# Optimization experiments

Measured on AMD Instinct MI355X. Metric: run time of the kernel, lower is better.

The kernel has to match this reference:

```python
import jax, jax.numpy as jnp
import numpy as np

N = 2_097_152  # number of pose pairs


def _skew(w):
    # w: [N,3] -> [N,3,3] skew-symmetric matrices
    x, y, z = w[..., 0], w[..., 1], w[..., 2]
    O = jnp.zeros_like(x)
    return jnp.stack([
        jnp.stack([O, -z, y], -1),
        jnp.stack([z, O, -x], -1),
        jnp.stack([-y, x, O], -1),
    ], -2)


def _exp_se3(xi):
    # xi: [N,6] twist = [rot_vec(3), trans(3)] -> (R:[N,3,3], t:[N,3])
    w, v = xi[..., :3], xi[..., 3:]
    t2 = jnp.sum(w * w, -1)                      # theta^2
    small = t2 < 1e-8
    t2s = jnp.where(small, 1.0, t2)              # safe denominator
    th = jnp.sqrt(t2s)
    A = jnp.where(small, 1.0 - t2 / 6.0, jnp.sin(th) / th)
    B = jnp.where(small, 0.5 - t2 / 24.0, (1.0 - jnp.cos(th)) / t2s)
    C = jnp.where(small, 1.0 / 6.0 - t2 / 120.0, (th - jnp.sin(th)) / (t2s * th))
    K = _skew(w)
    K2 = K @ K
    I = jnp.eye(3, dtype=xi.dtype)
    R = I + A[..., None, None] * K + B[..., None, None] * K2
    V = I + B[..., None, None] * K + C[..., None, None] * K2
    t = jnp.einsum('nij,nj->ni', V, v)
    return R, t


def _log_se3(R, t):
    # SE(3) log map: (R:[N,3,3], t:[N,3]) -> (w:[N,3], v:[N,3])
    tr = R[..., 0, 0] + R[..., 1, 1] + R[..., 2, 2]
    c = jnp.clip((tr - 1.0) * 0.5, -1.0 + 1e-7, 1.0 - 1e-7)
    th = jnp.arccos(c)
    small = th < 1e-4
    s = jnp.sin(th)
    ths = jnp.where(small, 1.0, th)
    ss = jnp.where(small, 1.0, s)
    coef = jnp.where(small, 0.5 + th * th / 12.0, th / (2.0 * ss))
    wvec = coef[..., None] * jnp.stack([
        R[..., 2, 1] - R[..., 1, 2],
        R[..., 0, 2] - R[..., 2, 0],
        R[..., 1, 0] - R[..., 0, 1],
    ], -1)
    K = _skew(wvec)
    K2 = K @ K
    one_m_c = jnp.where(small, 1.0, 1.0 - c)
    D = jnp.where(small, 1.0 / 12.0,
                  (1.0 - th * s / (2.0 * one_m_c)) / (ths * ths))
    I = jnp.eye(3, dtype=R.dtype)
    Vinv = I - 0.5 * K + D[..., None, None] * K2
    vvec = jnp.einsum('nij,nj->ni', Vinv, t)
    return wvec, vvec


def setup_inputs() -> dict:
    key = jax.random.key(0)
    k1, k2 = jax.random.split(key)
    predict = jax.random.normal(k1, (N, 6), dtype=jnp.float32)
    target = jax.random.normal(k2, (N, 6), dtype=jnp.float32)
    return {"predict": predict, "target": target}


def reference(predict, target):
    # per-sample SE(3) geodesic loss, reduction='mean'
    Rp, tp = _exp_se3(predict)
    Rt, tt = _exp_se3(target)
    # relative transform T_pred^{-1} T_target
    Rd = jnp.einsum('nji,njk->nik', Rp, Rt)           # Rp^T @ Rt
    td = jnp.einsum('nji,nj->ni', Rp, tt - tp)        # Rp^T (tt - tp)
    w, v = _log_se3(Rd, td)
    loss = jnp.sum(w * w, -1) + jnp.sum(v * v, -1)    # squared twist norm [N]
    return jnp.mean(loss)
```

## Files before the change

kernel.cpp:

```cpp
#include <hip/hip_runtime.h>

#define BLOCK 256
#define GRID  2048

__device__ __forceinline__ float frcp(float x) { return __builtin_amdgcn_rcpf(x); }

__device__ __forceinline__ void expse3(float wx, float wy, float wz,
                                       float vx, float vy, float vz,
                                       float* R, float* t)
{
    float t2 = wx*wx + wy*wy + wz*wz;
    bool  sm = t2 < 1e-8f;
    float t2s = sm ? 1.0f : t2;
    float th  = sqrtf(t2s);
    float s, c;
    __sincosf(th, &s, &c);
    float rth  = frcp(th);
    float rt2s = rth * rth;
    float A = sm ? 1.0f - t2*(1.0f/6.0f)                 : s * rth;
    float B = sm ? 0.5f - t2*(1.0f/24.0f)                : (1.0f - c) * rt2s;
    float C = sm ? (1.0f/6.0f) - t2*(1.0f/120.0f)        : (1.0f - s*rth) * rt2s;
    float Bxy = B*wx*wy, Bxz = B*wx*wz, Byz = B*wy*wz;
    R[0] = 1.0f + B*(wx*wx - t2); R[1] = Bxy - A*wz;            R[2] = Bxz + A*wy;
    R[3] = Bxy + A*wz;            R[4] = 1.0f + B*(wy*wy - t2); R[5] = Byz - A*wx;
    R[6] = Bxz - A*wy;            R[7] = Byz + A*wx;            R[8] = 1.0f + B*(wz*wz - t2);
    float Cxy = C*wx*wy, Cxz = C*wx*wz, Cyz = C*wy*wz;
    float V0 = 1.0f + C*(wx*wx - t2), V1 = Cxy - B*wz,            V2 = Cxz + B*wy;
    float V3 = Cxy + B*wz,            V4 = 1.0f + C*(wy*wy - t2), V5 = Cyz - B*wx;
    float V6 = Cxz - B*wy,            V7 = Cyz + B*wx,            V8 = 1.0f + C*(wz*wz - t2);
    t[0] = V0*vx + V1*vy + V2*vz;
    t[1] = V3*vx + V4*vy + V5*vz;
    t[2] = V6*vx + V7*vy + V8*vz;
}

__global__ void __launch_bounds__(BLOCK)
se3_loss_kernel(const float* __restrict__ pred, const float* __restrict__ targ,
                float* __restrict__ out, int n, float invN)
{
    float acc = 0.0f;
    int stride = gridDim.x * blockDim.x;
    for (int i = blockIdx.x * blockDim.x + threadIdx.x; i < n; i += stride) {
        const float2* p2 = reinterpret_cast<const float2*>(pred) + 3 * (size_t)i;
        const float2* q2 = reinterpret_cast<const float2*>(targ) + 3 * (size_t)i;
        float2 pa = p2[0], pb = p2[1], pc = p2[2];
        float2 qa = q2[0], qb = q2[1], qc = q2[2];

        float Rp[9], tp[3], Rt[9], tt[3];
        expse3(pa.x, pa.y, pb.x, pb.y, pc.x, pc.y, Rp, tp);
        expse3(qa.x, qa.y, qb.x, qb.y, qc.x, qc.y, Rt, tt);

        float d0 = tt[0] - tp[0], d1 = tt[1] - tp[1], d2 = tt[2] - tp[2];
        float Rd[9];
        #pragma unroll
        for (int ii = 0; ii < 3; ii++)
            #pragma unroll
            for (int kk = 0; kk < 3; kk++)
                Rd[ii*3+kk] = Rp[0+ii]*Rt[0+kk] + Rp[3+ii]*Rt[3+kk] + Rp[6+ii]*Rt[6+kk];
        float td0 = Rp[0]*d0 + Rp[3]*d1 + Rp[6]*d2;
        float td1 = Rp[1]*d0 + Rp[4]*d1 + Rp[7]*d2;
        float td2 = Rp[2]*d0 + Rp[5]*d1 + Rp[8]*d2;

        float tr = Rd[0] + Rd[4] + Rd[8];
        float c  = fminf(fmaxf((tr - 1.0f) * 0.5f, -1.0f + 1e-7f), 1.0f - 1e-7f);
        float th = acosf(c);
        bool  sm = th < 1e-4f;
        float s  = __sinf(th);
        float ths = sm ? 1.0f : th;
        float ss  = sm ? 1.0f : s;
        float coef = sm ? 0.5f + th*th*(1.0f/12.0f) : th * 0.5f * frcp(ss);
        float wx = coef * (Rd[7] - Rd[5]);
        float wy = coef * (Rd[2] - Rd[6]);
        float wz = coef * (Rd[3] - Rd[1]);
        float w2 = wx*wx + wy*wy + wz*wz;
        float omc = sm ? 1.0f : 1.0f - c;
        float rths = frcp(ths);
        float D = sm ? (1.0f/12.0f)
                     : (1.0f - th*s*0.5f*frcp(omc)) * rths * rths;
        float Dxy = D*wx*wy, Dxz = D*wx*wz, Dyz = D*wy*wz;
        float Vi0 = 1.0f + D*(wx*wx - w2), Vi1 =  0.5f*wz + Dxy,           Vi2 = -0.5f*wy + Dxz;
        float Vi3 = -0.5f*wz + Dxy,        Vi4 = 1.0f + D*(wy*wy - w2),    Vi5 =  0.5f*wx + Dyz;
        float Vi6 =  0.5f*wy + Dxz,        Vi7 = -0.5f*wx + Dyz,           Vi8 = 1.0f + D*(wz*wz - w2);
        float vx = Vi0*td0 + Vi1*td1 + Vi2*td2;
        float vy = Vi3*td0 + Vi4*td1 + Vi5*td2;
        float vz = Vi6*td0 + Vi7*td1 + Vi8*td2;

        acc += w2 + vx*vx + vy*vy + vz*vz;
    }

    #pragma unroll
    for (int off = 32; off; off >>= 1) acc += __shfl_down(acc, off, 64);
    __shared__ float wsum[BLOCK / 64];
    int lane = threadIdx.x & 63, wid = threadIdx.x >> 6;
    if (lane == 0) wsum[wid] = acc;
    __syncthreads();
    if (threadIdx.x == 0) {
        float s = 0.0f;
        #pragma unroll
        for (int k = 0; k < BLOCK / 64; k++) s += wsum[k];
        atomicAdd(out, s * invN);
    }
}

extern "C" void kernel_launch(void* const* d_in, const int* in_sizes, int n_in,
                              void* d_out, int out_size, void* d_ws, size_t ws_size,
                              hipStream_t stream) {
    const float* pred = (const float*)d_in[0];
    const float* targ = (const float*)d_in[1];
    float* out = (float*)d_out;
    int n = in_sizes[0] / 6;
    hipMemsetAsync(out, 0, (size_t)out_size * sizeof(float), stream);
    se3_loss_kernel<<<GRID, BLOCK, 0, stream>>>(pred, targ, out, n, 1.0f / (float)n);
}
```

Baseline: 128.6 us.

## Use float4 loads, two rows per thread, and polynomial acos approximation

Each thread now handles two pose pairs, read with three float4 loads per input instead of float2 loads, and the grid covers all pairs with no grid-stride loop. acosf is replaced by a short polynomial approximation, sin(theta) is derived from sqrt(1-c^2), and the small-angle branches in the log map are removed. The exp map uses raw hardware sqrt and explicit fmas. The intent is to cut transcendental and select cost and improve load width. In exchange it adds approximation error, drops the small-angle handling (possible loss of accuracy near theta=0), and silently ignores an odd final row.

```diff
diff --git a/kernel.cpp b/kernel.cpp
--- a/kernel.cpp
+++ b/kernel.cpp
@@ -1,25 +1,34 @@
 #include <hip/hip_runtime.h>
 
 #define BLOCK 256
-#define GRID  2048
 
-__device__ __forceinline__ float frcp(float x) { return __builtin_amdgcn_rcpf(x); }
+__device__ __forceinline__ float frcp(float x)  { return __builtin_amdgcn_rcpf(x); }
+__device__ __forceinline__ float fsqrt_(float x){ return __builtin_amdgcn_sqrtf(x); }
+
+__device__ __forceinline__ float facos(float x) {
+    float a = fabsf(x);
+    float p = fmaf(a, -0.0187293f, 0.0742610f);
+    p = fmaf(a, p, -0.2121144f);
+    p = fmaf(a, p, 1.5707288f);
+    float r = fsqrt_(1.0f - a) * p;
+    return x < 0.0f ? 3.14159265358979f - r : r;
+}
 
 __device__ __forceinline__ void expse3(float wx, float wy, float wz,
                                        float vx, float vy, float vz,
                                        float* R, float* t)
 {
-    float t2 = wx*wx + wy*wy + wz*wz;
+    float t2 = fmaf(wx, wx, fmaf(wy, wy, wz * wz));
     bool  sm = t2 < 1e-8f;
     float t2s = sm ? 1.0f : t2;
-    float th  = sqrtf(t2s);
+    float th  = fsqrt_(t2s);
     float s, c;
     __sincosf(th, &s, &c);
     float rth  = frcp(th);
-    float rt2s = rth * rth;
-    float A = sm ? 1.0f - t2*(1.0f/6.0f)                 : s * rth;
-    float B = sm ? 0.5f - t2*(1.0f/24.0f)                : (1.0f - c) * rt2s;
-    float C = sm ? (1.0f/6.0f) - t2*(1.0f/120.0f)        : (1.0f - s*rth) * rt2s;
+    float rt2  = rth * rth;
+    float A = sm ? fmaf(t2, -1.0f/6.0f,   1.0f)      : s * rth;
+    float B = sm ? fmaf(t2, -1.0f/24.0f,  0.5f)      : (1.0f - c) * rt2;
+    float C = sm ? fmaf(t2, -1.0f/120.0f, 1.0f/6.0f) : (1.0f - s * rth) * rt2;
     float Bxy = B*wx*wy, Bxz = B*wx*wz, Byz = B*wy*wz;
     R[0] = 1.0f + B*(wx*wx - t2); R[1] = Bxy - A*wz;            R[2] = Bxz + A*wy;
     R[3] = Bxy + A*wz;            R[4] = 1.0f + B*(wy*wy - t2); R[5] = Byz - A*wx;
@@ -33,58 +42,61 @@
     t[2] = V6*vx + V7*vy + V8*vz;
 }
 
+__device__ __forceinline__ float row_loss(
+    float pwx, float pwy, float pwz, float pvx, float pvy, float pvz,
+    float qwx, float qwy, float qwz, float qvx, float qvy, float qvz)
+{
+    float Rp[9], tp[3], Rt[9], tt[3];
+    expse3(pwx, pwy, pwz, pvx, pvy, pvz, Rp, tp);
+    expse3(qwx, qwy, qwz, qvx, qvy, qvz, Rt, tt);
+
+    float d0 = tt[0] - tp[0], d1 = tt[1] - tp[1], d2 = tt[2] - tp[2];
+    float Rd[9];
+    #pragma unroll
+    for (int ii = 0; ii < 3; ii++)
+        #pragma unroll
+        for (int kk = 0; kk < 3; kk++)
+            Rd[ii*3+kk] = Rp[0+ii]*Rt[0+kk] + Rp[3+ii]*Rt[3+kk] + Rp[6+ii]*Rt[6+kk];
+    float td0 = Rp[0]*d0 + Rp[3]*d1 + Rp[6]*d2;
+    float td1 = Rp[1]*d0 + Rp[4]*d1 + Rp[7]*d2;
+    float td2 = Rp[2]*d0 + Rp[5]*d1 + Rp[8]*d2;
+
+    float tr = Rd[0] + Rd[4] + Rd[8];
+    float c  = fminf(fmaxf((tr - 1.0f) * 0.5f, -1.0f + 1e-7f), 1.0f - 1e-7f);
+    float th = facos(c);
+    float s  = fsqrt_(fmaxf(1.0f - c*c, 0.0f));
+    float coef = th * 0.5f * frcp(s);
+    float wx = coef * (Rd[7] - Rd[5]);
+    float wy = coef * (Rd[2] - Rd[6]);
+    float wz = coef * (Rd[3] - Rd[1]);
+    float w2 = fmaf(wx, wx, fmaf(wy, wy, wz * wz));
+    float rth = frcp(th);
+    float D = (1.0f - th * s * 0.5f * frcp(1.0f - c)) * rth * rth;
+    float Dxy = D*wx*wy, Dxz = D*wx*wz, Dyz = D*wy*wz;
+    float Vi0 = 1.0f + D*(wx*wx - w2), Vi1 =  0.5f*wz + Dxy,           Vi2 = -0.5f*wy + Dxz;
+    float Vi3 = -0.5f*wz + Dxy,        Vi4 = 1.0f + D*(wy*wy - w2),    Vi5 =  0.5f*wx + Dyz;
+    float Vi6 =  0.5f*wy + Dxz,        Vi7 = -0.5f*wx + Dyz,           Vi8 = 1.0f + D*(wz*wz - w2);
+    float vx = Vi0*td0 + Vi1*td1 + Vi2*td2;
+    float vy = Vi3*td0 + Vi4*td1 + Vi5*td2;
+    float vz = Vi6*td0 + Vi7*td1 + Vi8*td2;
+
+    return w2 + fmaf(vx, vx, fmaf(vy, vy, vz * vz));
+}
+
 __global__ void __launch_bounds__(BLOCK)
-se3_loss_kernel(const float* __restrict__ pred, const float* __restrict__ targ,
-                float* __restrict__ out, int n, float invN)
+se3_loss_kernel(const float4* __restrict__ pred, const float4* __restrict__ targ,
+                float* __restrict__ out, int npair, float invN)
 {
+    int tid = blockIdx.x * BLOCK + threadIdx.x;
     float acc = 0.0f;
-    int stride = gridDim.x * blockDim.x;
-    for (int i = blockIdx.x * blockDim.x + threadIdx.x; i < n; i += stride) {
-        const float2* p2 = reinterpret_cast<const float2*>(pred) + 3 * (size_t)i;
-        const float2* q2 = reinterpret_cast<const float2*>(targ) + 3 * (size_t)i;
-        float2 pa = p2[0], pb = p2[1], pc = p2[2];
-        float2 qa = q2[0], qb = q2[1], qc = q2[2];
-
-        float Rp[9], tp[3], Rt[9], tt[3];
-        expse3(pa.x, pa.y, pb.x, pb.y, pc.x, pc.y, Rp, tp);
-        expse3(qa.x, qa.y, qb.x, qb.y, qc.x, qc.y, Rt, tt);
-
-        float d0 = tt[0] - tp[0], d1 = tt[1] - tp[1], d2 = tt[2] - tp[2];
-        float Rd[9];
-        #pragma unroll
-        for (int ii = 0; ii < 3; ii++)
-            #pragma unroll
-            for (int kk = 0; kk < 3; kk++)
-                Rd[ii*3+kk] = Rp[0+ii]*Rt[0+kk] + Rp[3+ii]*Rt[3+kk] + Rp[6+ii]*Rt[6+kk];
-        float td0 = Rp[0]*d0 + Rp[3]*d1 + Rp[6]*d2;
-        float td1 = Rp[1]*d0 + Rp[4]*d1 + Rp[7]*d2;
-        float td2 = Rp[2]*d0 + Rp[5]*d1 + Rp[8]*d2;
-
-        float tr = Rd[0] + Rd[4] + Rd[8];
-        float c  = fminf(fmaxf((tr - 1.0f) * 0.5f, -1.0f + 1e-7f), 1.0f - 1e-7f);
-        float th = acosf(c);
-        bool  sm = th < 1e-4f;
-        float s  = __sinf(th);
-        float ths = sm ? 1.0f : th;
-        float ss  = sm ? 1.0f : s;
-        float coef = sm ? 0.5f + th*th*(1.0f/12.0f) : th * 0.5f * frcp(ss);
-        float wx = coef * (Rd[7] - Rd[5]);
-        float wy = coef * (Rd[2] - Rd[6]);
-        float wz = coef * (Rd[3] - Rd[1]);
-        float w2 = wx*wx + wy*wy + wz*wz;
-        float omc = sm ? 1.0f : 1.0f - c;
-        float rths = frcp(ths);
-        float D = sm ? (1.0f/12.0f)
-                     : (1.0f - th*s*0.5f*frcp(omc)) * rths * rths;
-        float Dxy = D*wx*wy, Dxz = D*wx*wz, Dyz = D*wy*wz;
-        float Vi0 = 1.0f + D*(wx*wx - w2), Vi1 =  0.5f*wz + Dxy,           Vi2 = -0.5f*wy + Dxz;
-        float Vi3 = -0.5f*wz + Dxy,        Vi4 = 1.0f + D*(wy*wy - w2),    Vi5 =  0.5f*wx + Dyz;
-        float Vi6 =  0.5f*wy + Dxz,        Vi7 = -0.5f*wx + Dyz,           Vi8 = 1.0f + D*(wz*wz - w2);
-        float vx = Vi0*td0 + Vi1*td1 + Vi2*td2;
-        float vy = Vi3*td0 + Vi4*td1 + Vi5*td2;
-        float vz = Vi6*td0 + Vi7*td1 + Vi8*td2;
-
-        acc += w2 + vx*vx + vy*vy + vz*vz;
+    if (tid < npair) {
+        size_t b = 3 * (size_t)tid;
+        float4 p0 = pred[b], p1 = pred[b+1], p2 = pred[b+2];
+        float4 q0 = targ[b], q1 = targ[b+1], q2 = targ[b+2];
+        acc  = row_loss(p0.x,p0.y,p0.z, p0.w,p1.x,p1.y,
+                        q0.x,q0.y,q0.z, q0.w,q1.x,q1.y);
+        acc += row_loss(p1.z,p1.w,p2.x, p2.y,p2.z,p2.w,
+                        q1.z,q1.w,q2.x, q2.y,q2.z,q2.w);
     }
 
     #pragma unroll
@@ -104,10 +116,13 @@
 extern "C" void kernel_launch(void* const* d_in, const int* in_sizes, int n_in,
                               void* d_out, int out_size, void* d_ws, size_t ws_size,
                               hipStream_t stream) {
-    const float* pred = (const float*)d_in[0];
-    const float* targ = (const float*)d_in[1];
+    const float4* pred = (const float4*)d_in[0];
+    const float4* targ = (const float4*)d_in[1];
     float* out = (float*)d_out;
     int n = in_sizes[0] / 6;
+    int npair = n / 2;
+    int grid = (npair + BLOCK - 1) / BLOCK;
     hipMemsetAsync(out, 0, (size_t)out_size * sizeof(float), stream);
-    se3_loss_kernel<<<GRID, BLOCK, 0, stream>>>(pred, targ, out, n, 1.0f / (float)n);
+    se3_loss_kernel<<<grid, BLOCK, 0, stream>>>(pred, targ, out, npair,
+                                                1.0f / (float)n);
 }
```

Result: slower. 151.2 us (+17.6%).
